# Performance work log

Measured on AMD Instinct MI355X. Metric: run time of the kernel, lower is better.

Reference implementation:

```python
import jax, jax.numpy as jnp
import numpy as np

V = 196608   # HEALPix nside=128 -> 12*128^2 pixels
NNZ = 1769472  # ~9 entries per row (8 neighbors + diagonal)
B = 4
P = 64
Q = 64
K = 3  # KERNEL_SIZE


def setup_inputs() -> dict:
    key = jax.random.key(0)
    ks = jax.random.split(key, 5)
    return {
        "lap_vals": jax.random.normal(ks[0], (NNZ,), jnp.float32) * 0.1,
        "x": jax.random.normal(ks[1], (B, V, P), jnp.float32),
        "weight": jax.random.normal(ks[2], (K, P, Q), jnp.float32) * 0.1,
        "bias": jnp.full((Q,), 0.01, jnp.float32),
        "lap_rows": jax.random.randint(ks[3], (NNZ,), 0, V, jnp.int32),
        "lap_cols": jax.random.randint(ks[4], (NNZ,), 0, V, jnp.int32),
    }


def _spmm(vals, rows, cols, x):
    # sparse [V,V] @ dense [V,M] via gather + segment_sum
    return jax.ops.segment_sum(vals[:, None] * x[cols], rows, num_segments=V)


def reference(lap_vals, x, weight, bias, lap_rows, lap_cols):
    Bb, Vv, Pp = x.shape
    Kk, _, Qq = weight.shape
    # x0: [V, P*B] as in torch permute(1,2,0).view
    x0 = x.transpose(1, 2, 0).reshape(Vv, Pp * Bb)
    x1 = _spmm(lap_vals, lap_rows, lap_cols, x0)
    x2 = 2.0 * _spmm(lap_vals, lap_rows, lap_cols, x1) - x0
    cheb = jnp.stack([x0, x1, x2], 0).reshape(Kk, Vv, Pp, Bb)  # [K,V,P,B]
    inp = cheb.transpose(3, 1, 2, 0).reshape(Bb * Vv, Pp * Kk)  # [B*V, P*K]
    # NOTE: weight [K,P,Q] flattened C-order to [K*P, Q], matching torch .view
    out = inp @ weight.reshape(Kk * Pp, Qq)
    return out.reshape(Bb, Vv, Qq) + bias
```

## Files before the change

### kernel.cpp

```cpp
#include <hip/hip_runtime.h>
#include <hip/hip_bf16.h>

#define Vn   196608
#define NNZn 1769472
#define Bn   4
#define Pn   64
#define Qn   64
#define VPn  (Vn*Pn)

typedef __hip_bfloat16 bf16;
typedef __attribute__((ext_vector_type(8))) short bf16x8;
typedef __attribute__((ext_vector_type(4))) float f32x4;
typedef __attribute__((ext_vector_type(4))) unsigned int u32x4;

__device__ inline short f2bs(float f){
  __hip_bfloat16 h = __float2bfloat16(f);
  return *(short*)&h;
}
__device__ inline float lo16(unsigned u){ return __uint_as_float(u<<16); }
__device__ inline float hi16(unsigned u){ return __uint_as_float(u & 0xffff0000u); }


__global__ void k_zero(unsigned* __restrict__ p, int n){
  int i = blockIdx.x*blockDim.x + threadIdx.x;
  if(i<n) p[i]=0u;
}


__global__ void k_pre(const int* __restrict__ rows, unsigned* __restrict__ counts,
                      const float* __restrict__ x, short* __restrict__ x0c,
                      const float* __restrict__ wf, short* __restrict__ wcb){
  const int bid = blockIdx.x;
  int h=-1, f=-1;
  if(bid < 25920){
    if(bid%15==0) h = bid/15;
    else          f = 14*(bid/15) + (bid%15) - 1;
  } else {
    f = 24192 + (bid - 25920);
  }
  if(h >= 0){
    const int i = (h*256 + threadIdx.x)*4;
    const int4 r = *(const int4*)(rows + i);
    atomicAdd(&counts[r.x], 1u);
    atomicAdd(&counts[r.y], 1u);
    atomicAdd(&counts[r.z], 1u);
    atomicAdd(&counts[r.w], 1u);
  } else if(f < 24576){
    const int i = f*256 + threadIdx.x;
    const int o = i*8;
    const int v = o>>8, bp = o&255;
    const int hh = bp>>7, w7 = bp&127;
    const int b = (hh<<1) + (w7>>6), p = w7&63;
    const float* xp = x + (size_t)b*VPn + (size_t)v*64 + p;
    const float4 f0 = *(const float4*)xp;
    const float4 f1 = *(const float4*)(xp+4);
    unsigned r0 = ((unsigned)(unsigned short)f2bs(f0.y)<<16) | (unsigned)(unsigned short)f2bs(f0.x);
    unsigned r1 = ((unsigned)(unsigned short)f2bs(f0.w)<<16) | (unsigned)(unsigned short)f2bs(f0.z);
    unsigned r2 = ((unsigned)(unsigned short)f2bs(f1.y)<<16) | (unsigned)(unsigned short)f2bs(f1.x);
    unsigned r3 = ((unsigned)(unsigned short)f2bs(f1.w)<<16) | (unsigned)(unsigned short)f2bs(f1.z);
    u32x4 u; u[0]=r0; u[1]=r1; u[2]=r2; u[3]=r3;
    *(u32x4*)(x0c + ((size_t)hh*Vn + v)*128 + w7) = u;
  } else {
    const int idx = (f - 24576)*256 + threadIdx.x;
    const int q = idx/192, rem = idx%192, part = rem>>6, p = rem&63;
    float w;
    if(part==0)      w = wf[(3*p+0)*64+q] - wf[(3*p+2)*64+q];
    else if(part==1) w = wf[(3*p+1)*64+q];
    else             w = 2.0f*wf[(3*p+2)*64+q];
    wcb[idx] = f2bs(w);
  }
}

__global__ __launch_bounds__(1024) void k_scan_block(const unsigned* __restrict__ counts,
                                                     unsigned* __restrict__ incl,
                                                     unsigned* __restrict__ bsums){
  __shared__ unsigned s[1024];
  const int tid = threadIdx.x;
  const int gid = blockIdx.x*1024 + tid;
  s[tid] = counts[gid];
  __syncthreads();
  for(int off=1; off<1024; off<<=1){
    unsigned v = (tid>=off) ? s[tid-off] : 0u;
    __syncthreads();
    s[tid] += v;
    __syncthreads();
  }
  incl[gid] = s[tid];
  if(tid==1023) bsums[blockIdx.x] = s[1023];
}

__global__ void k_scan_top(unsigned* __restrict__ bs){
  __shared__ unsigned t[192];
  const int i = threadIdx.x;
  if(i<192) t[i]=bs[i];
  __syncthreads();
  for(int off=1; off<192; off<<=1){
    unsigned v = (i>=off && i<192) ? t[i-off] : 0u;
    __syncthreads();
    if(i<192) t[i] += v;
    __syncthreads();
  }
  if(i<192) bs[i] = (i==0) ? 0u : t[i-1];
}

__global__ void k_scan_add(const unsigned* __restrict__ counts, unsigned* __restrict__ incl,
                           const unsigned* __restrict__ boffs,
                           unsigned* __restrict__ rstart, unsigned* __restrict__ cursor){
  int i = blockIdx.x*blockDim.x + threadIdx.x;
  unsigned e = incl[i] + boffs[i>>10];
  incl[i] = e;
  unsigned st = e - counts[i];
  rstart[i] = st;
  cursor[i] = st;
}

__global__ void k_scatter(const float* __restrict__ vals, const int* __restrict__ rows,
                          const int* __restrict__ cols, unsigned* __restrict__ cursor,
                          int2* __restrict__ meta){
  int i = blockIdx.x*blockDim.x + threadIdx.x;
  int r = rows[i];
  unsigned pos = atomicAdd(&cursor[r], 1u);
  int2 m; m.x = cols[i]; m.y = __float_as_int(vals[i]);
  meta[pos] = m;
}


#define SP_STAGE(U,W,I) { int c_=0; float wv_=0.f; \
    if((I) < n){ const int2 m_ = meta[s+(unsigned)(I)]; c_=m_.x; wv_=__int_as_float(m_.y);} \
    W = wv_; U = *(const u32x4*)(src + (size_t)c_*SROW + off); }
#define SP_CONSUME(U,W) { \
    a0=fmaf(W,lo16(U[0]),a0); a1=fmaf(W,hi16(U[0]),a1); \
    a2=fmaf(W,lo16(U[1]),a2); a3=fmaf(W,hi16(U[1]),a3); \
    a4=fmaf(W,lo16(U[2]),a4); a5=fmaf(W,hi16(U[2]),a5); \
    a6=fmaf(W,lo16(U[3]),a6); a7=fmaf(W,hi16(U[3]),a7); }
#define SP_BODY \
  float a0=0,a1=0,a2=0,a3=0,a4=0,a5=0,a6=0,a7=0; \
  if(nmax > 0){ \
    u32x4 u0,u1,u2,u3; float w0,w1,w2,w3; \
    SP_STAGE(u0,w0,0) SP_STAGE(u1,w1,1) SP_STAGE(u2,w2,2) SP_STAGE(u3,w3,3) \
    int rem = nmax - 4; \
    int j = 4; \
    while(rem > 0){ \
      const u32x4 p0=u0, p1=u1, p2=u2, p3=u3; \
      const float q0=w0, q1=w1, q2=w2, q3=w3; \
      SP_STAGE(u0,w0,j) SP_STAGE(u1,w1,j+1) SP_STAGE(u2,w2,j+2) SP_STAGE(u3,w3,j+3) \
      SP_CONSUME(p0,q0) SP_CONSUME(p1,q1) SP_CONSUME(p2,q2) SP_CONSUME(p3,q3) \
      rem -= 4; j += 4; \
    } \
    SP_CONSUME(u0,w0) SP_CONSUME(u1,w1) SP_CONSUME(u2,w2) SP_CONSUME(u3,w3) \
  } \
  unsigned r0 = ((unsigned)(unsigned short)f2bs(a1)<<16) | (unsigned)(unsigned short)f2bs(a0); \
  unsigned r1 = ((unsigned)(unsigned short)f2bs(a3)<<16) | (unsigned)(unsigned short)f2bs(a2); \
  unsigned r2 = ((unsigned)(unsigned short)f2bs(a5)<<16) | (unsigned)(unsigned short)f2bs(a4); \
  unsigned r3 = ((unsigned)(unsigned short)f2bs(a7)<<16) | (unsigned)(unsigned short)f2bs(a6); \
  u32x4 ov; ov[0]=r0; ov[1]=r1; ov[2]=r2; ov[3]=r3;

template<int SROW, size_t PSTR>
__global__ __launch_bounds__(256) void k_spmm(const short* __restrict__ src,
                          const int2* __restrict__ meta,
                          const unsigned* __restrict__ rstart, const unsigned* __restrict__ rend,
                          short* __restrict__ dst){
  const int tid = threadIdx.x;
  const int lane = tid & 63;
  const int half = lane >> 5, sub = lane & 31;
  const int vbase = blockIdx.x*8 + (tid>>6)*2;
  const unsigned sA = rstart[vbase],   sB = rstart[vbase+1];
  const int nA = (int)(rend[vbase]-sA), nB = (int)(rend[vbase+1]-sB);
  const int nmax = (nA > nB) ? nA : nB;
  const unsigned s = half ? sB : sA;
  const int n = half ? nB : nA;
  const size_t off = (size_t)(sub>>4)*PSTR + (size_t)((sub&15)*8);
  SP_BODY
  *(u32x4*)(dst + (size_t)(vbase+half)*256 + sub*8) = ov;
}


__global__ __launch_bounds__(256) void k_gemm_fused(
    const short* __restrict__ x0, const short* __restrict__ x1,
    const short* __restrict__ wcb, const float* __restrict__ bias,
    const int2* __restrict__ meta, const unsigned* __restrict__ rstart,
    const unsigned* __restrict__ rend, float* __restrict__ out){
  __shared__ short ylds[4][16*264];
  const int t = threadIdx.x, w = t>>6, l = t&63;
  const int half = l>>5, sub = l&31;
  const int vw = blockIdx.x*64 + w*16;
  short* const my = &ylds[w][0];
  const short* const src = x1;
  const int SROW = 256;
  const size_t off = (size_t)(sub>>4)*128 + (size_t)((sub&15)*8);

  for(int pr=0; pr<8; ++pr){
    const int vb = vw + pr*2;
    const unsigned sA = rstart[vb], sB = rstart[vb+1];
    const int nA = (int)(rend[vb]-sA), nB = (int)(rend[vb+1]-sB);
    const int nmax = (nA > nB) ? nA : nB;
    const unsigned s = half ? sB : sA;
    const int n = half ? nB : nA;
    SP_BODY
    *(u32x4*)(my + (pr*2+half)*264 + off) = ov;
  }

  const int r = l&15, g = l>>4;
  f32x4 acc[4][4] = {};
#pragma unroll
  for(int c=0; c<6; ++c){
    const int part = c>>1, ko = (c&1)*32;
    const int kw = part*64 + ko + 8*g;
    const bf16x8 bfr0 = *(const bf16x8*)&wcb[( 0+r)*192 + kw];
    const bf16x8 bfr1 = *(const bf16x8*)&wcb[(16+r)*192 + kw];
    const bf16x8 bfr2 = *(const bf16x8*)&wcb[(32+r)*192 + kw];
    const bf16x8 bfr3 = *(const bf16x8*)&wcb[(48+r)*192 + kw];
#pragma unroll
    for(int bb=0; bb<4; ++bb){
      bf16x8 a;
      if(part==0)      a = *(const bf16x8*)(x0 + ((size_t)(bb>>1)*Vn + vw + r)*128 + (bb&1)*64 + ko + 8*g);
      else if(part==1) a = *(const bf16x8*)(x1 + ((size_t)(vw + r))*256 + bb*64 + ko + 8*g);
      else             a = *(const bf16x8*)(my + r*264 + bb*64 + ko + 8*g);
      acc[bb][0] = __builtin_amdgcn_mfma_f32_16x16x32_bf16(a, bfr0, acc[bb][0], 0, 0, 0);
      acc[bb][1] = __builtin_amdgcn_mfma_f32_16x16x32_bf16(a, bfr1, acc[bb][1], 0, 0, 0);
      acc[bb][2] = __builtin_amdgcn_mfma_f32_16x16x32_bf16(a, bfr2, acc[bb][2], 0, 0, 0);
      acc[bb][3] = __builtin_amdgcn_mfma_f32_16x16x32_bf16(a, bfr3, acc[bb][3], 0, 0, 0);
    }
  }

#pragma unroll
  for(int bb=0; bb<4; ++bb){
    float* ob = out + (size_t)bb*Vn*64;
#pragma unroll
    for(int n=0; n<4; ++n){
      const float bq = bias[n*16+r];
#pragma unroll
      for(int reg=0; reg<4; ++reg)
        ob[(size_t)(vw + g*4 + reg)*64 + n*16 + r] = acc[bb][n][reg] + bq;
    }
  }
}


extern "C" void kernel_launch(void* const* d_in, const int* in_sizes, int n_in,
                              void* d_out, int out_size, void* d_ws, size_t ws_size,
                              hipStream_t stream){
  const float* lap_vals = (const float*)d_in[0];
  const float* x        = (const float*)d_in[1];
  const float* weight   = (const float*)d_in[2];
  const float* bias     = (const float*)d_in[3];
  const int*   lap_rows = (const int*)d_in[4];
  const int*   lap_cols = (const int*)d_in[5];
  float* out = (float*)d_out;
  short* x0c = (short*)d_out;

  char* w = (char*)d_ws;
  short* x1b = (short*)w;          w += (size_t)Vn*256*sizeof(short);
  int2* meta = (int2*)w;           w += (size_t)NNZn*8;
  unsigned* counts = (unsigned*)w; w += (size_t)Vn*4;
  unsigned* cursor = (unsigned*)w; w += (size_t)Vn*4;
  unsigned* rstart = (unsigned*)w; w += (size_t)Vn*4;
  unsigned* rend   = (unsigned*)w; w += (size_t)Vn*4;
  unsigned* bsums  = (unsigned*)w; w += 1024;
  short* wcb = (short*)w;          w += 12288*sizeof(short);

  k_zero<<<Vn/256, 256, 0, stream>>>(counts, Vn);
  k_pre<<<26352, 256, 0, stream>>>(lap_rows, counts, x, x0c, weight, wcb);
  k_scan_block<<<192, 1024, 0, stream>>>(counts, rend, bsums);
  k_scan_top<<<1, 256, 0, stream>>>(bsums);
  k_scan_add<<<Vn/256, 256, 0, stream>>>(counts, rend, bsums, rstart, cursor);
  k_scatter<<<NNZn/256, 256, 0, stream>>>(lap_vals, lap_rows, lap_cols, cursor, meta);

  k_spmm<128, (size_t)Vn*128><<<Vn/8, 256, 0, stream>>>(x0c, meta, rstart, rend, x1b);

  k_gemm_fused<<<Vn/64, 256, 0, stream>>>(x0c, x1b, wcb, bias,
                                          meta, rstart, rend, out);
}
```

Baseline: 610.0 us.

## Build CSR via two-level bucket sort instead of global per-row atomics

Replaces the COO-to-CSR construction. It drops the per-row global atomic histogram, the three-kernel scan and the global-atomic scatter. In their place is a two-pass bucket sort: a coarse histogram over 256 row buckets of 768 rows each, built with shared-memory atomics, a single-block scan, a bucketing pass that writes row and meta entries per bucket, and a per-bucket CSR kernel that counts, scans and scatters locally in shared memory. This is meant to cut contended global atomics and scattered global writes, at the cost of an extra intermediate buffer pass and only 256 blocks in the final CSR step.

```diff
diff --git a/kernel.cpp b/kernel.cpp
--- a/kernel.cpp
+++ b/kernel.cpp
@@ -7,6 +7,10 @@
 #define Pn   64
 #define Qn   64
 #define VPn  (Vn*Pn)
+#define NB   256
+#define RPB  768
+#define EPT  4096
+#define NTIL 432
 
 typedef __hip_bfloat16 bf16;
 typedef __attribute__((ext_vector_type(8))) short bf16x8;
@@ -20,33 +24,34 @@
 __device__ inline float lo16(unsigned u){ return __uint_as_float(u<<16); }
 __device__ inline float hi16(unsigned u){ return __uint_as_float(u & 0xffff0000u); }
 
-
-__global__ void k_zero(unsigned* __restrict__ p, int n){
-  int i = blockIdx.x*blockDim.x + threadIdx.x;
-  if(i<n) p[i]=0u;
-}
-
-
-__global__ void k_pre(const int* __restrict__ rows, unsigned* __restrict__ counts,
+__global__ void k_zero256(unsigned* __restrict__ g){ g[threadIdx.x] = 0u; }
+
+
+__global__ __launch_bounds__(256) void k_pre(const int* __restrict__ rows, unsigned* __restrict__ gcount,
                       const float* __restrict__ x, short* __restrict__ x0c,
                       const float* __restrict__ wf, short* __restrict__ wcb){
-  const int bid = blockIdx.x;
-  int h=-1, f=-1;
-  if(bid < 25920){
-    if(bid%15==0) h = bid/15;
-    else          f = 14*(bid/15) + (bid%15) - 1;
-  } else {
-    f = 24192 + (bid - 25920);
-  }
-  if(h >= 0){
-    const int i = (h*256 + threadIdx.x)*4;
-    const int4 r = *(const int4*)(rows + i);
-    atomicAdd(&counts[r.x], 1u);
-    atomicAdd(&counts[r.y], 1u);
-    atomicAdd(&counts[r.z], 1u);
-    atomicAdd(&counts[r.w], 1u);
-  } else if(f < 24576){
-    const int i = f*256 + threadIdx.x;
+  __shared__ unsigned hcnt[NB];
+  const int bid = blockIdx.x, t = threadIdx.x;
+  if(bid % 58 == 0){
+    const int cb = bid/58;
+    hcnt[t] = 0u;
+    __syncthreads();
+    const int base = cb*EPT;
+#pragma unroll
+    for(int k=0;k<4;++k){
+      const int4 r = *(const int4*)(rows + base + k*1024 + t*4);
+      atomicAdd(&hcnt[(unsigned)r.x/RPB], 1u);
+      atomicAdd(&hcnt[(unsigned)r.y/RPB], 1u);
+      atomicAdd(&hcnt[(unsigned)r.z/RPB], 1u);
+      atomicAdd(&hcnt[(unsigned)r.w/RPB], 1u);
+    }
+    __syncthreads();
+    atomicAdd(&gcount[t], hcnt[t]);
+    return;
+  }
+  const int f = bid - bid/58 - 1;
+  if(f < 24576){
+    const int i = f*256 + t;
     const int o = i*8;
     const int v = o>>8, bp = o&255;
     const int hh = bp>>7, w7 = bp&127;
@@ -61,7 +66,7 @@
     u32x4 u; u[0]=r0; u[1]=r1; u[2]=r2; u[3]=r3;
     *(u32x4*)(x0c + ((size_t)hh*Vn + v)*128 + w7) = u;
   } else {
-    const int idx = (f - 24576)*256 + threadIdx.x;
+    const int idx = (f - 24576)*256 + t;
     const int q = idx/192, rem = idx%192, part = rem>>6, p = rem&63;
     float w;
     if(part==0)      w = wf[(3*p+0)*64+q] - wf[(3*p+2)*64+q];
@@ -71,57 +76,98 @@
   }
 }
 
-__global__ __launch_bounds__(1024) void k_scan_block(const unsigned* __restrict__ counts,
-                                                     unsigned* __restrict__ incl,
-                                                     unsigned* __restrict__ bsums){
-  __shared__ unsigned s[1024];
-  const int tid = threadIdx.x;
-  const int gid = blockIdx.x*1024 + tid;
-  s[tid] = counts[gid];
-  __syncthreads();
-  for(int off=1; off<1024; off<<=1){
-    unsigned v = (tid>=off) ? s[tid-off] : 0u;
-    __syncthreads();
-    s[tid] += v;
-    __syncthreads();
-  }
-  incl[gid] = s[tid];
-  if(tid==1023) bsums[blockIdx.x] = s[1023];
-}
-
-__global__ void k_scan_top(unsigned* __restrict__ bs){
-  __shared__ unsigned t[192];
+__global__ void k_scan256(const unsigned* __restrict__ gcount, unsigned* __restrict__ gbase,
+                          unsigned* __restrict__ gcursor){
+  __shared__ unsigned t[NB];
   const int i = threadIdx.x;
-  if(i<192) t[i]=bs[i];
-  __syncthreads();
-  for(int off=1; off<192; off<<=1){
-    unsigned v = (i>=off && i<192) ? t[i-off] : 0u;
-    __syncthreads();
-    if(i<192) t[i] += v;
-    __syncthreads();
-  }
-  if(i<192) bs[i] = (i==0) ? 0u : t[i-1];
-}
-
-__global__ void k_scan_add(const unsigned* __restrict__ counts, unsigned* __restrict__ incl,
-                           const unsigned* __restrict__ boffs,
-                           unsigned* __restrict__ rstart, unsigned* __restrict__ cursor){
-  int i = blockIdx.x*blockDim.x + threadIdx.x;
-  unsigned e = incl[i] + boffs[i>>10];
-  incl[i] = e;
-  unsigned st = e - counts[i];
-  rstart[i] = st;
-  cursor[i] = st;
-}
-
-__global__ void k_scatter(const float* __restrict__ vals, const int* __restrict__ rows,
-                          const int* __restrict__ cols, unsigned* __restrict__ cursor,
-                          int2* __restrict__ meta){
-  int i = blockIdx.x*blockDim.x + threadIdx.x;
-  int r = rows[i];
-  unsigned pos = atomicAdd(&cursor[r], 1u);
-  int2 m; m.x = cols[i]; m.y = __float_as_int(vals[i]);
-  meta[pos] = m;
+  const unsigned c = gcount[i];
+  t[i] = c;
+  __syncthreads();
+  for(int off=1; off<NB; off<<=1){
+    unsigned v = (i>=off) ? t[i-off] : 0u;
+    __syncthreads();
+    t[i] += v;
+    __syncthreads();
+  }
+  const unsigned excl = t[i] - c;
+  gbase[i] = excl;
+  gcursor[i] = excl;
+  if(i == NB-1) gbase[NB] = t[NB-1];
+}
+
+__global__ __launch_bounds__(256) void k_bucket(const int* __restrict__ rows, const int* __restrict__ cols,
+                         const float* __restrict__ vals, unsigned* __restrict__ gcursor,
+                         int* __restrict__ brow, int2* __restrict__ bmeta){
+  __shared__ unsigned hcnt[NB];
+  __shared__ unsigned lcur[NB];
+  const int t = threadIdx.x;
+  const int base = blockIdx.x*EPT;
+  hcnt[t] = 0u;
+  __syncthreads();
+  int4 r4[4];
+#pragma unroll
+  for(int k=0;k<4;++k){
+    r4[k] = *(const int4*)(rows + base + k*1024 + t*4);
+    atomicAdd(&hcnt[(unsigned)r4[k].x/RPB], 1u);
+    atomicAdd(&hcnt[(unsigned)r4[k].y/RPB], 1u);
+    atomicAdd(&hcnt[(unsigned)r4[k].z/RPB], 1u);
+    atomicAdd(&hcnt[(unsigned)r4[k].w/RPB], 1u);
+  }
+  __syncthreads();
+  lcur[t] = atomicAdd(&gcursor[t], hcnt[t]);
+  __syncthreads();
+#pragma unroll
+  for(int k=0;k<4;++k){
+    const int4   c4 = *(const int4*)(cols + base + k*1024 + t*4);
+    const float4 v4 = *(const float4*)(vals + base + k*1024 + t*4);
+    unsigned p;
+    p = atomicAdd(&lcur[(unsigned)r4[k].x/RPB],1u); brow[p]=r4[k].x; { int2 m; m.x=c4.x; m.y=__float_as_int(v4.x); bmeta[p]=m; }
+    p = atomicAdd(&lcur[(unsigned)r4[k].y/RPB],1u); brow[p]=r4[k].y; { int2 m; m.x=c4.y; m.y=__float_as_int(v4.y); bmeta[p]=m; }
+    p = atomicAdd(&lcur[(unsigned)r4[k].z/RPB],1u); brow[p]=r4[k].z; { int2 m; m.x=c4.z; m.y=__float_as_int(v4.z); bmeta[p]=m; }
+    p = atomicAdd(&lcur[(unsigned)r4[k].w/RPB],1u); brow[p]=r4[k].w; { int2 m; m.x=c4.w; m.y=__float_as_int(v4.w); bmeta[p]=m; }
+  }
+}
+
+__global__ __launch_bounds__(256) void k_csr(const int* __restrict__ brow, const int2* __restrict__ bmeta,
+                      const unsigned* __restrict__ gbase,
+                      unsigned* __restrict__ rstart, unsigned* __restrict__ rend,
+                      int2* __restrict__ meta){
+  __shared__ unsigned rcnt[RPB];
+  __shared__ unsigned rcur[RPB];
+  __shared__ unsigned ssum[256];
+  const int t = threadIdx.x, b = blockIdx.x;
+  const unsigned base = gbase[b];
+  const int nb = (int)(gbase[b+1] - base);
+  const int rv0 = b*RPB;
+#pragma unroll
+  for(int k=0;k<3;++k) rcnt[t*3+k] = 0u;
+  __syncthreads();
+  for(int e=t; e<nb; e+=256){
+    const int r = brow[base+e] - rv0;
+    atomicAdd(&rcnt[r], 1u);
+  }
+  __syncthreads();
+  const unsigned c0 = rcnt[t*3], c1 = rcnt[t*3+1], c2 = rcnt[t*3+2];
+  const unsigned mysum = c0+c1+c2;
+  ssum[t] = mysum;
+  __syncthreads();
+  for(int off=1; off<256; off<<=1){
+    unsigned v = (t>=off) ? ssum[t-off] : 0u;
+    __syncthreads();
+    ssum[t] += v;
+    __syncthreads();
+  }
+  const unsigned excl = ssum[t] - mysum;
+  const unsigned s0 = base + excl, s1 = s0 + c0, s2 = s1 + c1;
+  rstart[rv0+t*3+0] = s0;  rend[rv0+t*3+0] = s0 + c0;  rcur[t*3+0] = s0;
+  rstart[rv0+t*3+1] = s1;  rend[rv0+t*3+1] = s1 + c1;  rcur[t*3+1] = s1;
+  rstart[rv0+t*3+2] = s2;  rend[rv0+t*3+2] = s2 + c2;  rcur[t*3+2] = s2;
+  __syncthreads();
+  for(int e=t; e<nb; e+=256){
+    const int r = brow[base+e] - rv0;
+    const unsigned pos = atomicAdd(&rcur[r], 1u);
+    meta[pos] = bmeta[base+e];
+  }
 }
 
 
@@ -155,6 +201,7 @@
   unsigned r3 = ((unsigned)(unsigned short)f2bs(a7)<<16) | (unsigned)(unsigned short)f2bs(a6); \
   u32x4 ov; ov[0]=r0; ov[1]=r1; ov[2]=r2; ov[3]=r3;
 
+
 template<int SROW, size_t PSTR>
 __global__ __launch_bounds__(256) void k_spmm(const short* __restrict__ src,
                           const int2* __restrict__ meta,
@@ -252,19 +299,20 @@
   char* w = (char*)d_ws;
   short* x1b = (short*)w;          w += (size_t)Vn*256*sizeof(short);
   int2* meta = (int2*)w;           w += (size_t)NNZn*8;
-  unsigned* counts = (unsigned*)w; w += (size_t)Vn*4;
-  unsigned* cursor = (unsigned*)w; w += (size_t)Vn*4;
+  int2* bmeta = (int2*)w;          w += (size_t)NNZn*8;
+  int*  brow = (int*)w;            w += (size_t)NNZn*4;
   unsigned* rstart = (unsigned*)w; w += (size_t)Vn*4;
   unsigned* rend   = (unsigned*)w; w += (size_t)Vn*4;
-  unsigned* bsums  = (unsigned*)w; w += 1024;
+  unsigned* gcount = (unsigned*)w; w += NB*4;
+  unsigned* gbase  = (unsigned*)w; w += (NB+1)*4;
+  unsigned* gcursor= (unsigned*)w; w += NB*4;
   short* wcb = (short*)w;          w += 12288*sizeof(short);
 
-  k_zero<<<Vn/256, 256, 0, stream>>>(counts, Vn);
-  k_pre<<<26352, 256, 0, stream>>>(lap_rows, counts, x, x0c, weight, wcb);
-  k_scan_block<<<192, 1024, 0, stream>>>(counts, rend, bsums);
-  k_scan_top<<<1, 256, 0, stream>>>(bsums);
-  k_scan_add<<<Vn/256, 256, 0, stream>>>(counts, rend, bsums, rstart, cursor);
-  k_scatter<<<NNZn/256, 256, 0, stream>>>(lap_vals, lap_rows, lap_cols, cursor, meta);
+  k_zero256<<<1, 256, 0, stream>>>(gcount);
+  k_pre<<<25056, 256, 0, stream>>>(lap_rows, gcount, x, x0c, weight, wcb);
+  k_scan256<<<1, 256, 0, stream>>>(gcount, gbase, gcursor);
+  k_bucket<<<NTIL, 256, 0, stream>>>(lap_rows, lap_cols, lap_vals, gcursor, brow, bmeta);
+  k_csr<<<NB, 256, 0, stream>>>(brow, bmeta, gbase, rstart, rend, meta);
 
   k_spmm<128, (size_t)Vn*128><<<Vn/8, 256, 0, stream>>>(x0c, meta, rstart, rend, x1b);
 
```

After: 526.0 us. 13.8% less time.
